# Kernel tuning notes

Hardware: AMD Instinct MI355X
Metric: run time of the kernel (lower is better)

## Reference

```python
import jax, jax.numpy as jnp
import numpy as np

B, N, D, H, L, EXP = 8, 1024, 256, 8, 6, 4
TEMP = 1.0
LN_EPS = 1e-5


def setup_inputs() -> dict:
    key = jax.random.key(0)
    ks = jax.random.split(key, 16)
    s = 0.02  # param init scale
    return {
        "x": jax.random.normal(ks[0], (B, N, D), dtype=jnp.float32),
        "cls_token": jax.random.normal(ks[1], (1, 1, D), dtype=jnp.float32) * s,
        "dict_token": jax.random.normal(ks[2], (1, 1, D), dtype=jnp.float32) * s,
        "ln1_g": jnp.ones((L, D), jnp.float32),
        "ln1_b": jnp.zeros((L, D), jnp.float32),
        "qkv_w": jax.random.normal(ks[3], (L, D, H * D * 3), dtype=jnp.float32) * s,
        "qkv_b": jnp.zeros((L, H * D * 3), jnp.float32),
        "proj_w": jax.random.normal(ks[4], (L, H * D, D), dtype=jnp.float32) * s,
        "proj_b": jnp.zeros((L, D), jnp.float32),
        "ln2_g": jnp.ones((L, D), jnp.float32),
        "ln2_b": jnp.zeros((L, D), jnp.float32),
        "mlp_w1": jax.random.normal(ks[5], (L, D, EXP * D), dtype=jnp.float32) * s,
        "mlp_b1": jnp.zeros((L, EXP * D), jnp.float32),
        "mlp_w2": jax.random.normal(ks[6], (L, EXP * D, D), dtype=jnp.float32) * s,
        "mlp_b2": jnp.zeros((L, D), jnp.float32),
    }


def _layer_norm(y, g, b):
    m = y.mean(-1, keepdims=True)
    v = y.var(-1, keepdims=True)  # ddof=0 matches torch LayerNorm
    return (y - m) * jax.lax.rsqrt(v + LN_EPS) * g + b


def _forward(x, cls_token, dict_token, ln1_g, ln1_b, qkv_w, qkv_b, proj_w, proj_b,
             ln2_g, ln2_b, mlp_w1, mlp_b1, mlp_w2, mlp_b2):
    b, n, d = x.shape
    h = jnp.concatenate(
        [x,
         jnp.broadcast_to(cls_token, (b, 1, d)),
         jnp.broadcast_to(dict_token, (b, 1, d))], axis=1)  # [B, N+2, D]
    inv_sqrt_d = 1.0 / (d ** 0.5)

    def block(h, p):
        g1, b1, qw, qb, pw, pb, g2, b2, w1, c1, w2, c2 = p
        # NOTE: no residual connections in the source module
        h = _layer_norm(h, g1, b1)
        t = h.shape[1]
        qkv = (h @ qw + qb).reshape(b, t, H, d, 3)  # out index = h*(d*3)+f*3+c
        q = qkv[..., 0] * inv_sqrt_d  # [B, T, H, D]
        k = qkv[..., 1] * inv_sqrt_d
        v = qkv[..., 2]
        scores = jnp.einsum('bthd,bshd->bhts', q, k) / TEMP
        w = jax.nn.softmax(scores, axis=-1)
        o = jnp.einsum('bhts,bshd->bthd', w, v).reshape(b, t, H * d)
        h = o @ pw + pb
        h = _layer_norm(h, g2, b2)
        h = jax.nn.gelu(h @ w1 + c1, approximate=False)
        h = jax.nn.gelu(h @ w2 + c2, approximate=False)  # apply_activation_last=True
        return h, None

    h, _ = jax.lax.scan(block, h, (ln1_g, ln1_b, qkv_w, qkv_b, proj_w, proj_b,
                                   ln2_g, ln2_b, mlp_w1, mlp_b1, mlp_w2, mlp_b2))
    return h[:, :-2, :], h[:, -2:-1, :], h[:, -1:, :]


def reference(x, cls_token, dict_token, ln1_g, ln1_b, qkv_w, qkv_b, proj_w, proj_b,
              ln2_g, ln2_b, mlp_w1, mlp_b1, mlp_w2, mlp_b2):
    return _forward(x, cls_token, dict_token, ln1_g, ln1_b, qkv_w, qkv_b, proj_w,
                    proj_b, ln2_g, ln2_b, mlp_w1, mlp_b1, mlp_w2, mlp_b2)
```

## Files before the change

kernel.cpp:

```cpp
#include <hip/hip_runtime.h>
#include <hip/hip_bf16.h>
#include <math.h>
#include <stdio.h>

typedef unsigned short u16;
typedef unsigned int u32;
typedef __attribute__((ext_vector_type(8))) short short8;
typedef __attribute__((ext_vector_type(4))) float float4v;
typedef __attribute__((ext_vector_type(4))) u32  uint4v;
typedef __attribute__((ext_vector_type(2))) u32  uint2v;

static __device__ __forceinline__ float bf2f(u16 u) {
    return __uint_as_float(((u32)u) << 16);
}
static __device__ __forceinline__ u16 f2bf(float f) {
    u32 x = __float_as_uint(f);
    x += 0x7FFFu + ((x >> 16) & 1u);
    return (u16)(x >> 16);
}
static __device__ __forceinline__ float gelu_exact(float x) {
    return 0.5f * x * (1.0f + erff(x * 0.70710678118654752f));
}

static __device__ __forceinline__ void gl2lds16(const u16* g, u16* l) {
    __builtin_amdgcn_global_load_lds(
        (const __attribute__((address_space(1))) u32*)g,
        (__attribute__((address_space(3))) u32*)l, 16, 0, 0);
}

static __device__ __forceinline__ void wait_lds() {
#if __has_builtin(__builtin_amdgcn_s_waitcnt)
    __builtin_amdgcn_s_waitcnt(0xC07F);
#else
    __syncthreads();
#endif
}

#define TPAD 1152
#define MPAD (8 * TPAD)

__global__ void detect_k(const u32* __restrict__ x, u32* __restrict__ flag) {
    __shared__ int cnt;
    if (threadIdx.x == 0) cnt = 0;
    __syncthreads();
    u32 w = x[threadIdx.x];
    int e = (w >> 7) & 0xFF;
    if (e >= 108 && e <= 134) atomicAdd(&cnt, 1);
    __syncthreads();
    if (threadIdx.x == 0) *flag = (cnt > 128) ? 1u : 0u;
}

__global__ void convert_k(const void* __restrict__ src, u16* __restrict__ dst,
                          long n, const u32* __restrict__ flag) {
    long i = (long)blockIdx.x * 256 + threadIdx.x;
    if (i >= n) return;
    if (*flag) dst[i] = ((const u16*)src)[i];
    else       dst[i] = f2bf(((const float*)src)[i]);
}

__global__ void transposeT_k(const void* __restrict__ src, u16* __restrict__ dst,
                             int R, int C, int mode, const u32* __restrict__ flag) {
    __shared__ u16 t[32][33];
    int c0 = blockIdx.x * 32, r0 = blockIdx.y * 32;
    long lb = (long)blockIdx.z * R * C;
    int tx = threadIdx.x, ty = threadIdx.y;
    bool isbf = (*flag != 0);
    #pragma unroll
    for (int j = 0; j < 4; ++j) {
        long idx = lb + (long)(r0 + ty + j * 8) * C + (c0 + tx);
        t[ty + j * 8][tx] = isbf ? ((const u16*)src)[idx]
                                 : f2bf(((const float*)src)[idx]);
    }
    __syncthreads();
    #pragma unroll
    for (int j = 0; j < 4; ++j) {
        int c = c0 + ty + j * 8;
        int n = (mode == 1) ? ((c % 3) * 2048 + (c / 768) * 256 + ((c % 768) / 3)) : c;
        dst[lb + (long)n * R + (r0 + tx)] = t[tx][ty + j * 8];
    }
}

__global__ void qkvbias_k(const void* __restrict__ src, u16* __restrict__ dst,
                          const u32* __restrict__ flag) {
    int i = blockIdx.x * 256 + threadIdx.x;
    int l = i / 6144, n = i % 6144;
    float v = *flag ? bf2f(((const u16*)src)[i]) : ((const float*)src)[i];
    int np = (n % 3) * 2048 + (n / 768) * 256 + ((n % 768) / 3);
    dst[l * 6144 + np] = f2bf(v);
}

struct GP {
    const u16 *A, *B, *bias;
    void* C;
    u16 *q, *k, *v;
    long sA, sB, sC;
    int M, N, K, ldC;
    int epi, zoff;
};

#define RPS 136

template <int BM, int BN>
__global__ __launch_bounds__(256) void gemmNT_k(GP p) {
    constexpr int MI = BM / 32, NI = BN / 32;
    __shared__ __align__(16) u16 smem[(BM + BN) * 64];
    u16* As = smem;
    u16* Bs = smem + BM * 64;

    const int tid  = threadIdx.x;
    const int lane = tid & 63, wave = tid >> 6;
    const int wr = wave >> 1, wc = wave & 1;
    const int lrow = lane & 15, quad = lane >> 4;
    const int bn0 = blockIdx.x * BN, bm0 = blockIdx.y * BM, bz = blockIdx.z;
    const u16* A = p.A + (long)bz * p.sA;
    const u16* B = p.B + (long)bz * p.sB;
    const int srow = lane >> 3, schk = lane & 7;
    const int sq = ((schk ^ srow) << 3);
    const int K = p.K;

    float4v acc[MI][NI] = {};

    for (int k0 = 0; k0 < K; k0 += 64) {
        #pragma unroll
        for (int j = 0; j < BM / 32; ++j) {
            int m = j * 32 + wave * 8;
            gl2lds16(A + (long)(bm0 + m + srow) * K + k0 + sq, &As[m * 64]);
        }
        #pragma unroll
        for (int j = 0; j < BN / 32; ++j) {
            int n = j * 32 + wave * 8;
            gl2lds16(B + (long)(bn0 + n + srow) * K + k0 + sq, &Bs[n * 64]);
        }
        __syncthreads();

        #pragma unroll
        for (int s = 0; s < 2; ++s) {
            short8 af[MI], bfv[NI];
            #pragma unroll
            for (int mi = 0; mi < MI; ++mi) {
                int m = wr * (BM / 2) + mi * 16 + lrow;
                int c = (s * 4 + quad) ^ (m & 7);
                af[mi] = *(const short8*)&As[m * 64 + c * 8];
            }
            #pragma unroll
            for (int ni = 0; ni < NI; ++ni) {
                int n = wc * (BN / 2) + ni * 16 + lrow;
                int c = (s * 4 + quad) ^ (n & 7);
                bfv[ni] = *(const short8*)&Bs[n * 64 + c * 8];
            }
            #pragma unroll
            for (int mi = 0; mi < MI; ++mi)
                #pragma unroll
                for (int ni = 0; ni < NI; ++ni)
                    acc[mi][ni] = __builtin_amdgcn_mfma_f32_16x16x32_bf16(
                        af[mi], bfv[ni], acc[mi][ni], 0, 0, 0);
        }
        __syncthreads();
    }

    if constexpr (BM == 128 && BN == 128) {
        if (p.epi == 1 || p.epi == 3) {
            u16* rp = smem;
            const int c3 = (p.epi == 3) ? (bn0 >> 11) : -1;
            for (int ch = 0; ch < 2; ++ch) {
                if (wr == ch) {
                    #pragma unroll
                    for (int mi = 0; mi < MI; ++mi)
                        #pragma unroll
                        for (int ni = 0; ni < NI; ++ni)
                            #pragma unroll
                            for (int r = 0; r < 4; ++r) {
                                int lr = mi * 16 + quad * 4 + r;
                                int lc = wc * 64 + ni * 16 + lrow;
                                float val = acc[mi][ni][r];
                                if (p.epi == 3) {
                                    val += bf2f(p.bias[bn0 + lc]);
                                    if (c3 < 2) val *= 0.0625f;
                                } else {
                                    val = gelu_exact(val + bf2f(p.bias[bn0 + lc]));
                                }
                                rp[lr * RPS + lc] = f2bf(val);
                            }
                }
                __syncthreads();
                if (p.epi == 3 && c3 == 2) {
                    int head = (bn0 & 2047) >> 8, fb = bn0 & 255;
                    int bloc = bm0 / TPAD;
                    int tb = bm0 - bloc * TPAD + ch * 64;
                    long zb = bloc * 8 + head;
                    #pragma unroll
                    for (int pp = 0; pp < 4; ++pp) {
                        int f_l = pp * 32 + (tid >> 3);
                        int t8  = (tid & 7) * 8;
                        union { uint4v v; u16 e[8]; } o;
                        #pragma unroll
                        for (int j = 0; j < 8; ++j) o.e[j] = rp[(t8 + j) * RPS + f_l];
                        *(uint4v*)&p.v[(zb * 256 + fb + f_l) * (long)TPAD + tb + t8] = o.v;
                    }
                } else {
                    #pragma unroll
                    for (int pp = 0; pp < 4; ++pp) {
                        int row_l = pp * 16 + (tid >> 4);
                        int col8  = (tid & 15) * 8;
                        uint4v w = *(const uint4v*)&rp[row_l * RPS + col8];
                        int grow = bm0 + ch * 64 + row_l;
                        u16* base; long dst;
                        if (p.epi == 1) {
                            base = (u16*)p.C;
                            dst = (long)grow * 1024 + bn0 + col8;
                        } else {
                            int head = (bn0 & 2047) >> 8, fb = bn0 & 255;
                            int bloc = grow / TPAD, t = grow - bloc * TPAD;
                            base = (c3 == 0) ? p.q : p.k;
                            dst = ((long)(bloc * 8 + head) * TPAD + t) * 256 + fb + col8;
                        }
                        *(uint4v*)&base[dst] = w;
                    }
                }
                __syncthreads();
            }
            return;
        }
    }
    #pragma unroll
    for (int mi = 0; mi < MI; ++mi) {
        #pragma unroll
        for (int ni = 0; ni < NI; ++ni) {
            #pragma unroll
            for (int r = 0; r < 4; ++r) {
                int row = bm0 + wr * (BM / 2) + mi * 16 + quad * 4 + r;
                int col = bn0 + wc * (BN / 2) + ni * 16 + lrow;
                float v2 = acc[mi][ni][r] + bf2f(p.bias[col]);
                if (p.epi == 2) v2 = gelu_exact(v2);
                ((float*)p.C)[(long)row * p.ldC + col] = v2;
            }
        }
    }
}

__global__ __launch_bounds__(256) void flash_k(const u16* __restrict__ qb,
                                               const u16* __restrict__ kb,
                                               const u16* __restrict__ vT,
                                               u16* __restrict__ ao, int zoff) {
    __shared__ __align__(16) u16 smem[16384 + 16384 + 4608];
    u16* KR = smem;
    u16* VR = smem + 16384;

    const int tid  = threadIdx.x;
    const int lane = tid & 63, wave = tid >> 6;
    const int lrow = lane & 15, quad = lane >> 4;
    const int srow = lane >> 3, schk = lane & 7;
    const int sq   = ((schk ^ srow) << 3);
    const int q0   = blockIdx.x * 64;
    const int z    = blockIdx.y;
    u16* Plds = smem + 32768 + wave * (16 * 72);

    const u16* Qp = qb + ((long)z * TPAD + q0) * 256;
    const u16* Kp = kb + (long)z * TPAD * 256;
    const u16* Vp = vT + (long)z * 256 * TPAD;

    #pragma unroll
    for (int k0 = 0; k0 < 4; ++k0)
        #pragma unroll
        for (int j = 0; j < 2; ++j) {
            int m = j * 32 + wave * 8;
            gl2lds16(Qp + (long)(m + srow) * 256 + k0 * 64 + sq,
                     &KR[k0 * 4096 + m * 64]);
        }
    __syncthreads();
    const int mloc = wave * 16 + lrow;
    short8 qf[8];
    #pragma unroll
    for (int k0 = 0; k0 < 4; ++k0)
        #pragma unroll
        for (int s = 0; s < 2; ++s)
            qf[k0 * 2 + s] = *(const short8*)&KR[k0 * 4096 + mloc * 64
                            + (((s * 4 + quad) ^ (mloc & 7)) << 3)];
    __syncthreads();

    float4v Oacc[16] = {};
    float   lacc[4] = {};

    for (int kv = 0; kv < TPAD; kv += 64) {
        #pragma unroll
        for (int c = 0; c < 4; ++c)
            #pragma unroll
            for (int j = 0; j < 2; ++j) {
                int n = j * 32 + wave * 8;
                gl2lds16(Kp + (long)(kv + n + srow) * 256 + c * 64 + sq,
                         &KR[c * 4096 + n * 64]);
                gl2lds16(Vp + (long)(c * 64 + n + srow) * TPAD + kv + sq,
                         &VR[c * 4096 + n * 64]);
            }
        __syncthreads();

        float4v Sacc[4] = {};
        #pragma unroll
        for (int k0 = 0; k0 < 4; ++k0)
            #pragma unroll
            for (int s = 0; s < 2; ++s)
                #pragma unroll
                for (int ni = 0; ni < 4; ++ni) {
                    int n = ni * 16 + lrow;
                    short8 bf = *(const short8*)&KR[k0 * 4096 + n * 64
                                + (((s * 4 + quad) ^ (n & 7)) << 3)];
                    Sacc[ni] = __builtin_amdgcn_mfma_f32_16x16x32_bf16(
                        qf[k0 * 2 + s], bf, Sacc[ni], 0, 0, 0);
                }

        #pragma unroll
        for (int r = 0; r < 4; ++r) {
            float rs = 0.0f;
            #pragma unroll
            for (int ni = 0; ni < 4; ++ni) {
                int col = kv + ni * 16 + lrow;
                float e = (col < 1026) ? __expf(Sacc[ni][r]) : 0.0f;
                Plds[(quad * 4 + r) * 72 + ni * 16 + lrow] = f2bf(e);
                rs += e;
            }
            rs += __shfl_xor(rs, 1, 64);
            rs += __shfl_xor(rs, 2, 64);
            rs += __shfl_xor(rs, 4, 64);
            rs += __shfl_xor(rs, 8, 64);
            lacc[r] += rs;
        }
        wait_lds();

        #pragma unroll
        for (int dc = 0; dc < 4; ++dc)
            #pragma unroll
            for (int s = 0; s < 2; ++s) {
                short8 af = *(const short8*)&Plds[lrow * 72 + (s * 4 + quad) * 8];
                #pragma unroll
                for (int ni = 0; ni < 4; ++ni) {
                    int n = ni * 16 + lrow;
                    short8 bf = *(const short8*)&VR[dc * 4096 + n * 64
                                + (((s * 4 + quad) ^ (n & 7)) << 3)];
                    Oacc[dc * 4 + ni] = __builtin_amdgcn_mfma_f32_16x16x32_bf16(
                        af, bf, Oacc[dc * 4 + ni], 0, 0, 0);
                }
            }
        __syncthreads();
    }

    u16* out = smem;
    float inv[4];
    #pragma unroll
    for (int r = 0; r < 4; ++r) inv[r] = 1.0f / lacc[r];
    #pragma unroll
    for (int dc = 0; dc < 4; ++dc)
        #pragma unroll
        for (int ni = 0; ni < 4; ++ni)
            #pragma unroll
            for (int r = 0; r < 4; ++r) {
                int row = wave * 16 + quad * 4 + r;
                int col = dc * 64 + ni * 16 + lrow;
                out[row * 264 + col] = f2bf(Oacc[dc * 4 + ni][r] * inv[r]);
            }
    __syncthreads();
    int zg = zoff + z;
    int b = zg >> 3, head = zg & 7;
    #pragma unroll
    for (int pp = 0; pp < 8; ++pp) {
        int row  = pp * 8 + (tid >> 5);
        int col8 = (tid & 31) * 8;
        uint4v w = *(const uint4v*)&out[row * 264 + col8];
        *(uint4v*)&ao[((long)(b * TPAD) + q0 + row) * 2048 + head * 256 + col8] = w;
    }
}

__global__ __launch_bounds__(256) void ln_k(const float* __restrict__ h,
                                            const u16* __restrict__ g,
                                            const u16* __restrict__ b,
                                            u16* __restrict__ out, int M) {
    int row  = blockIdx.x * 4 + (threadIdx.x >> 6);
    int lane = threadIdx.x & 63;
    if (row >= M) return;
    const float* x = h + (long)row * 256;
    float4v v = *(const float4v*)(x + lane * 4);
    float s  = v[0] + v[1] + v[2] + v[3];
    float s2 = v[0] * v[0] + v[1] * v[1] + v[2] * v[2] + v[3] * v[3];
    #pragma unroll
    for (int off = 32; off; off >>= 1) {
        s  += __shfl_xor(s, off, 64);
        s2 += __shfl_xor(s2, off, 64);
    }
    float mean = s * (1.0f / 256.0f);
    float var  = s2 * (1.0f / 256.0f) - mean * mean;
    float rs   = rsqrtf(var + 1e-5f);
    union { uint2v v; u16 e[4]; } o;
    #pragma unroll
    for (int j = 0; j < 4; ++j) {
        int c = lane * 4 + j;
        o.e[j] = f2bf((v[j] - mean) * rs * bf2f(g[c]) + bf2f(b[c]));
    }
    *(uint2v*)&out[(long)row * 256 + lane * 4] = o.v;
}

__global__ void embed_k(const u16* __restrict__ x, const u16* __restrict__ cls,
                        const u16* __restrict__ dict, float* __restrict__ h) {
    long i = (long)blockIdx.x * 256 + threadIdx.x;
    int d = i & 255;
    long row = i >> 8;
    int b = (int)(row / TPAD), t = (int)(row - (long)b * TPAD);
    float v;
    if (t < 1024)       v = bf2f(x[((long)b * 1024 + t) * 256 + d]);
    else if (t == 1024) v = bf2f(cls[d]);
    else if (t == 1025) v = bf2f(dict[d]);
    else                v = 0.0f;
    h[i] = v;
}

__global__ void outconv_k(const float* __restrict__ h, void* __restrict__ out,
                          const u32* __restrict__ flag) {
    long i = (long)blockIdx.x * 256 + threadIdx.x;
    int d = i & 255;
    long row = i >> 8;
    int b = (int)(row / TPAD), t = (int)(row - (long)b * TPAD);
    long o;
    if (t < 1024)       o = ((long)b * 1024 + t) * 256 + d;
    else if (t == 1024) o = 8L * 1024 * 256 + (long)b * 256 + d;
    else if (t == 1025) o = 8L * 1024 * 256 + 8L * 256 + (long)b * 256 + d;
    else return;
    float v = h[i];
    if (*flag) ((u16*)out)[o] = f2bf(v);
    else       ((float*)out)[o] = v;
}

template <int BM, int BN>
static void launch_gemm(hipStream_t s, const GP& p, int nz) {
    dim3 grid(p.N / BN, p.M / BM, nz);
    gemmNT_k<BM, BN><<<grid, dim3(256), 0, s>>>(p);
}

extern "C" void kernel_launch(void* const* d_in, const int* in_sizes, int n_in,
                              void* d_out, int out_size, void* d_ws, size_t ws_size,
                              hipStream_t stream) {
    char* ws = (char*)d_ws;
    size_t used = 0;
    auto alloc = [&](size_t bytes) {
        char* ptr = ws + used;
        used += (bytes + 255) & ~(size_t)255;
        return ptr;
    };
    u32* flag = (u32*)alloc(256);

    static const int plainIdx[10] = {0, 1, 2, 3, 4, 8, 9, 10, 12, 14};
    u16* cp[15] = {};
    for (int j = 0; j < 10; ++j) {
        int i = plainIdx[j];
        cp[i] = (u16*)alloc((size_t)in_sizes[i] * 2);
    }
    u16* qkv_bP  = (u16*)alloc(6L * 6144 * 2);
    u16* qkv_wT  = (u16*)alloc(6L * 6144 * 256 * 2);
    u16* proj_wT = (u16*)alloc(6L * 256 * 2048 * 2);
    u16* w1T     = (u16*)alloc(6L * 1024 * 256 * 2);
    u16* w2T     = (u16*)alloc(6L * 256 * 1024 * 2);

    float* h  = (float*)alloc((size_t)MPAD * 256 * 4);
    u16*   hn = (u16*)  alloc((size_t)MPAD * 256 * 2);
    u16*   ao = (u16*)  alloc((size_t)MPAD * 2048 * 2);
    u16*   mid= (u16*)  alloc((size_t)MPAD * 1024 * 2);

    const size_t perB = (size_t)8 * 3L * TPAD * 256 * 2;
    int G = 8;
    while (G > 1 && used + (size_t)G * perB + 8192 > ws_size) G >>= 1;
    u16* qb = (u16*)alloc((size_t)G * 8 * TPAD * 256 * 2);
    u16* kb = (u16*)alloc((size_t)G * 8 * TPAD * 256 * 2);
    u16* vT = (u16*)alloc((size_t)G * 8 * 256 * TPAD * 2);
    if (used > ws_size) {
        fprintf(stderr, "kernel_launch: need %zu ws bytes, have %zu\n", used, ws_size);
        return;
    }

    detect_k<<<1, 256, 0, stream>>>((const u32*)d_in[0], flag);
    for (int j = 0; j < 10; ++j) {
        int i = plainIdx[j];
        long n = in_sizes[i];
        convert_k<<<(int)((n + 255) / 256), 256, 0, stream>>>(d_in[i], cp[i], n, flag);
    }
    qkvbias_k<<<6 * 6144 / 256, 256, 0, stream>>>(d_in[6], qkv_bP, flag);
    transposeT_k<<<dim3(6144/32, 256/32, 6), dim3(32, 8), 0, stream>>>(d_in[5],  qkv_wT,  256,  6144, 1, flag);
    transposeT_k<<<dim3(256/32, 2048/32, 6), dim3(32, 8), 0, stream>>>(d_in[7],  proj_wT, 2048, 256,  0, flag);
    transposeT_k<<<dim3(1024/32, 256/32, 6), dim3(32, 8), 0, stream>>>(d_in[11], w1T,     256,  1024, 0, flag);
    transposeT_k<<<dim3(256/32, 1024/32, 6), dim3(32, 8), 0, stream>>>(d_in[13], w2T,     1024, 256,  0, flag);

    embed_k<<<MPAD, 256, 0, stream>>>(cp[0], cp[1], cp[2], h);

    const int nGroups = 8 / G;
    for (int l = 0; l < 6; ++l) {
        ln_k<<<MPAD / 4, 256, 0, stream>>>(h, cp[3] + l * 256, cp[4] + l * 256, hn, MPAD);

        for (int g = 0; g < nGroups; ++g) {
            {
                GP p{};
                p.A = hn + (long)g * G * TPAD * 256;
                p.B = qkv_wT + (long)l * 6144 * 256;
                p.bias = qkv_bP + l * 6144;
                p.M = G * TPAD; p.N = 6144; p.K = 256;
                p.epi = 3; p.q = qb; p.k = kb; p.v = vT;
                launch_gemm<128, 128>(stream, p, 1);
            }
            flash_k<<<dim3(TPAD / 64, G * 8), dim3(256), 0, stream>>>(
                qb, kb, vT, ao, g * G * 8);
        }
        {
            GP p{};
            p.A = ao; p.B = proj_wT + (long)l * 256 * 2048;
            p.bias = cp[8] + l * 256;
            p.C = h; p.ldC = 256;
            p.M = MPAD; p.N = 256; p.K = 2048;
            p.epi = 0;
            launch_gemm<64, 64>(stream, p, 1);
        }
        ln_k<<<MPAD / 4, 256, 0, stream>>>(h, cp[9] + l * 256, cp[10] + l * 256, hn, MPAD);
        {
            GP p{};
            p.A = hn; p.B = w1T + (long)l * 1024 * 256;
            p.bias = cp[12] + l * 1024;
            p.C = mid;
            p.M = MPAD; p.N = 1024; p.K = 256;
            p.epi = 1;
            launch_gemm<128, 128>(stream, p, 1);
        }
        {
            GP p{};
            p.A = mid; p.B = w2T + (long)l * 256 * 1024;
            p.bias = cp[14] + l * 256;
            p.C = h; p.ldC = 256;
            p.M = MPAD; p.N = 256; p.K = 1024;
            p.epi = 2;
            launch_gemm<64, 64>(stream, p, 1);
        }
    }

    outconv_k<<<MPAD, 256, 0, stream>>>(h, d_out, flag);
}
```

Before: 2.256 ms.

## Retile flash attention into 2x2 wave grid with staggered K/V prefetch

The attention kernel now splits its 64x64 score and output tiles across a 2x2 wave grid. Each wave owns 32 query rows and half of the key columns (for scores) or half of the head dim (for output), so B fragments are reused across two M fragments. The next K tile is issued after the softmax step and the next V tile after the PV step, overlapping global loads with compute. Row sums from the two column waves are combined through LDS at the end. The launch also changes to a 1D grid that interleaves heads so neighbouring blocks share the same query tile index. This adds more barriers per iteration and a cross-wave reduction.

Measured after the change: 2.629 ms. +16.6%, slower.

```diff
diff --git a/kernel.cpp b/kernel.cpp
--- a/kernel.cpp
+++ b/kernel.cpp
@@ -26,14 +26,6 @@
     __builtin_amdgcn_global_load_lds(
         (const __attribute__((address_space(1))) u32*)g,
         (__attribute__((address_space(3))) u32*)l, 16, 0, 0);
-}
-
-static __device__ __forceinline__ void wait_lds() {
-#if __has_builtin(__builtin_amdgcn_s_waitcnt)
-    __builtin_amdgcn_s_waitcnt(0xC07F);
-#else
-    __syncthreads();
-#endif
 }
 
 #define TPAD 1152
@@ -242,18 +234,22 @@
                                                const u16* __restrict__ kb,
                                                const u16* __restrict__ vT,
                                                u16* __restrict__ ao, int zoff) {
-    __shared__ __align__(16) u16 smem[16384 + 16384 + 4608];
+    __shared__ __align__(16) u16 smem[16384 + 16384 + 4096];
     u16* KR = smem;
     u16* VR = smem + 16384;
 
     const int tid  = threadIdx.x;
     const int lane = tid & 63, wave = tid >> 6;
+    const int wr = wave >> 1, wc = wave & 1;
     const int lrow = lane & 15, quad = lane >> 4;
     const int srow = lane >> 3, schk = lane & 7;
     const int sq   = ((schk ^ srow) << 3);
-    const int q0   = blockIdx.x * 64;
-    const int z    = blockIdx.y;
-    u16* Plds = smem + 32768 + wave * (16 * 72);
+
+    const int blk = blockIdx.x;
+    const int t_  = blk >> 3;
+    const int q0  = (t_ % 18) * 64;
+    const int z   = (blk & 7) + 8 * (t_ / 18);
+    u16* Ph = smem + 32768 + wr * 2048;
 
     const u16* Qp = qb + ((long)z * TPAD + q0) * 256;
     const u16* Kp = kb + (long)z * TPAD * 256;
@@ -268,94 +264,148 @@
                      &KR[k0 * 4096 + m * 64]);
         }
     __syncthreads();
-    const int mloc = wave * 16 + lrow;
-    short8 qf[8];
-    #pragma unroll
-    for (int k0 = 0; k0 < 4; ++k0)
-        #pragma unroll
-        for (int s = 0; s < 2; ++s)
-            qf[k0 * 2 + s] = *(const short8*)&KR[k0 * 4096 + mloc * 64
-                            + (((s * 4 + quad) ^ (mloc & 7)) << 3)];
-    __syncthreads();
-
-    float4v Oacc[16] = {};
-    float   lacc[4] = {};
+    short8 qf[16];
+    #pragma unroll
+    for (int mi = 0; mi < 2; ++mi) {
+        int m = wr * 32 + mi * 16 + lrow;
+        #pragma unroll
+        for (int k0 = 0; k0 < 4; ++k0)
+            #pragma unroll
+            for (int s = 0; s < 2; ++s)
+                qf[mi * 8 + k0 * 2 + s] = *(const short8*)&KR[k0 * 4096 + m * 64
+                                + (((s * 4 + quad) ^ (m & 7)) << 3)];
+    }
+    __syncthreads();
+
+    #pragma unroll
+    for (int c = 0; c < 4; ++c)
+        #pragma unroll
+        for (int j = 0; j < 2; ++j) {
+            int n = j * 32 + wave * 8;
+            gl2lds16(Kp + (long)(n + srow) * 256 + c * 64 + sq,
+                     &KR[c * 4096 + n * 64]);
+            gl2lds16(Vp + (long)(c * 64 + n + srow) * TPAD + sq,
+                     &VR[c * 4096 + n * 64]);
+        }
+
+    float4v Oacc[2][8] = {};
+    float   lacc[8] = {};
 
     for (int kv = 0; kv < TPAD; kv += 64) {
-        #pragma unroll
-        for (int c = 0; c < 4; ++c)
-            #pragma unroll
-            for (int j = 0; j < 2; ++j) {
-                int n = j * 32 + wave * 8;
-                gl2lds16(Kp + (long)(kv + n + srow) * 256 + c * 64 + sq,
-                         &KR[c * 4096 + n * 64]);
-                gl2lds16(Vp + (long)(c * 64 + n + srow) * TPAD + kv + sq,
-                         &VR[c * 4096 + n * 64]);
-            }
         __syncthreads();
 
-        float4v Sacc[4] = {};
+        float4v Sacc[2][2] = {};
         #pragma unroll
         for (int k0 = 0; k0 < 4; ++k0)
             #pragma unroll
-            for (int s = 0; s < 2; ++s)
-                #pragma unroll
-                for (int ni = 0; ni < 4; ++ni) {
-                    int n = ni * 16 + lrow;
-                    short8 bf = *(const short8*)&KR[k0 * 4096 + n * 64
+            for (int s = 0; s < 2; ++s) {
+                short8 bfv[2];
+                #pragma unroll
+                for (int ni = 0; ni < 2; ++ni) {
+                    int n = wc * 32 + ni * 16 + lrow;
+                    bfv[ni] = *(const short8*)&KR[k0 * 4096 + n * 64
                                 + (((s * 4 + quad) ^ (n & 7)) << 3)];
-                    Sacc[ni] = __builtin_amdgcn_mfma_f32_16x16x32_bf16(
-                        qf[k0 * 2 + s], bf, Sacc[ni], 0, 0, 0);
-                }
-
+                }
+                #pragma unroll
+                for (int mi = 0; mi < 2; ++mi)
+                    #pragma unroll
+                    for (int ni = 0; ni < 2; ++ni)
+                        Sacc[mi][ni] = __builtin_amdgcn_mfma_f32_16x16x32_bf16(
+                            qf[mi * 8 + k0 * 2 + s], bfv[ni], Sacc[mi][ni], 0, 0, 0);
+            }
+
+        #pragma unroll
+        for (int mi = 0; mi < 2; ++mi)
+            #pragma unroll
+            for (int r = 0; r < 4; ++r) {
+                int rowL = mi * 16 + quad * 4 + r;
+                float rs = 0.0f;
+                #pragma unroll
+                for (int ni = 0; ni < 2; ++ni) {
+                    int colL = wc * 32 + ni * 16 + lrow;
+                    float e = (kv + colL < 1026) ? __expf(Sacc[mi][ni][r]) : 0.0f;
+                    int chunk = (colL >> 3) ^ (rowL & 7);
+                    Ph[rowL * 64 + chunk * 8 + (lrow & 7)] = f2bf(e);
+                    rs += e;
+                }
+                rs += __shfl_xor(rs, 1, 64);
+                rs += __shfl_xor(rs, 2, 64);
+                rs += __shfl_xor(rs, 4, 64);
+                rs += __shfl_xor(rs, 8, 64);
+                lacc[mi * 4 + r] += rs;
+            }
+        __syncthreads();
+
+        if (kv + 64 < TPAD) {
+            #pragma unroll
+            for (int c = 0; c < 4; ++c)
+                #pragma unroll
+                for (int j = 0; j < 2; ++j) {
+                    int n = j * 32 + wave * 8;
+                    gl2lds16(Kp + (long)(kv + 64 + n + srow) * 256 + c * 64 + sq,
+                             &KR[c * 4096 + n * 64]);
+                }
+        }
+
+        #pragma unroll
+        for (int w = 0; w < 2; ++w)
+            #pragma unroll
+            for (int mi = 0; mi < 2; ++mi) {
+                int rowL = mi * 16 + lrow;
+                short8 af = *(const short8*)&Ph[rowL * 64
+                            + (((w * 4 + quad) ^ (rowL & 7)) << 3)];
+                #pragma unroll
+                for (int ni = 0; ni < 8; ++ni) {
+                    int d = wc * 128 + ni * 16 + lrow;
+                    int c = d >> 6, dl = d & 63;
+                    short8 bf = *(const short8*)&VR[c * 4096 + dl * 64
+                                + (((w * 4 + quad) ^ (dl & 7)) << 3)];
+                    Oacc[mi][ni] = __builtin_amdgcn_mfma_f32_16x16x32_bf16(
+                        af, bf, Oacc[mi][ni], 0, 0, 0);
+                }
+            }
+        __syncthreads();
+
+        if (kv + 64 < TPAD) {
+            #pragma unroll
+            for (int c = 0; c < 4; ++c)
+                #pragma unroll
+                for (int j = 0; j < 2; ++j) {
+                    int n = j * 32 + wave * 8;
+                    gl2lds16(Vp + (long)(c * 64 + n + srow) * TPAD + kv + 64 + sq,
+                             &VR[c * 4096 + n * 64]);
+                }
+        }
+    }
+
+    float* Lex = (float*)(smem + 32768);
+    #pragma unroll
+    for (int mi = 0; mi < 2; ++mi)
         #pragma unroll
         for (int r = 0; r < 4; ++r) {
-            float rs = 0.0f;
-            #pragma unroll
-            for (int ni = 0; ni < 4; ++ni) {
-                int col = kv + ni * 16 + lrow;
-                float e = (col < 1026) ? __expf(Sacc[ni][r]) : 0.0f;
-                Plds[(quad * 4 + r) * 72 + ni * 16 + lrow] = f2bf(e);
-                rs += e;
-            }
-            rs += __shfl_xor(rs, 1, 64);
-            rs += __shfl_xor(rs, 2, 64);
-            rs += __shfl_xor(rs, 4, 64);
-            rs += __shfl_xor(rs, 8, 64);
-            lacc[r] += rs;
-        }
-        wait_lds();
-
-        #pragma unroll
-        for (int dc = 0; dc < 4; ++dc)
-            #pragma unroll
-            for (int s = 0; s < 2; ++s) {
-                short8 af = *(const short8*)&Plds[lrow * 72 + (s * 4 + quad) * 8];
-                #pragma unroll
-                for (int ni = 0; ni < 4; ++ni) {
-                    int n = ni * 16 + lrow;
-                    short8 bf = *(const short8*)&VR[dc * 4096 + n * 64
-                                + (((s * 4 + quad) ^ (n & 7)) << 3)];
-                    Oacc[dc * 4 + ni] = __builtin_amdgcn_mfma_f32_16x16x32_bf16(
-                        af, bf, Oacc[dc * 4 + ni], 0, 0, 0);
-                }
-            }
-        __syncthreads();
-    }
+            int row = wr * 32 + mi * 16 + quad * 4 + r;
+            if (lrow == 0) Lex[row * 2 + wc] = lacc[mi * 4 + r];
+        }
+    __syncthreads();
+    float linv[8];
+    #pragma unroll
+    for (int mi = 0; mi < 2; ++mi)
+        #pragma unroll
+        for (int r = 0; r < 4; ++r) {
+            int row = wr * 32 + mi * 16 + quad * 4 + r;
+            linv[mi * 4 + r] = 1.0f / (Lex[row * 2] + Lex[row * 2 + 1]);
+        }
 
     u16* out = smem;
-    float inv[4];
-    #pragma unroll
-    for (int r = 0; r < 4; ++r) inv[r] = 1.0f / lacc[r];
-    #pragma unroll
-    for (int dc = 0; dc < 4; ++dc)
-        #pragma unroll
-        for (int ni = 0; ni < 4; ++ni)
+    #pragma unroll
+    for (int mi = 0; mi < 2; ++mi)
+        #pragma unroll
+        for (int ni = 0; ni < 8; ++ni)
             #pragma unroll
             for (int r = 0; r < 4; ++r) {
-                int row = wave * 16 + quad * 4 + r;
-                int col = dc * 64 + ni * 16 + lrow;
-                out[row * 264 + col] = f2bf(Oacc[dc * 4 + ni][r] * inv[r]);
+                int row = wr * 32 + mi * 16 + quad * 4 + r;
+                int col = wc * 128 + ni * 16 + lrow;
+                out[row * 264 + col] = f2bf(Oacc[mi][ni][r] * linv[mi * 4 + r]);
             }
     __syncthreads();
     int zg = zoff + z;
@@ -501,7 +551,7 @@
                 p.epi = 3; p.q = qb; p.k = kb; p.v = vT;
                 launch_gemm<128, 128>(stream, p, 1);
             }
-            flash_k<<<dim3(TPAD / 64, G * 8), dim3(256), 0, stream>>>(
+            flash_k<<<dim3(18 * G * 8), dim3(256), 0, stream>>>(
                 qb, kb, vT, ao, g * G * 8);
         }
         {
```
